# Performance work log

Hardware: AMD Instinct MI355X
Metric: run time of the kernel (lower is better)

## Reference

```python
import jax, jax.numpy as jnp
import numpy as np


def setup_inputs() -> dict:
    key = jax.random.key(0)
    k1, k2 = jax.random.split(key)
    x = jax.random.normal(k1, (64, 3, 512, 512), dtype=jnp.float32)
    mean_params = jax.random.normal(k2, (64, 4), dtype=jnp.float32)
    return {"x": x, "mean_params": mean_params}


def _make_affine(mean_params):
    # 4-param branch: theta, scale, tx, ty -> [B, 2, 3] affine matrices
    theta = mean_params[:, 0]
    scale = mean_params[:, 1]
    tx = mean_params[:, 2]
    ty = mean_params[:, 3]
    ct = scale * jnp.cos(theta)
    st = scale * jnp.sin(theta)
    row0 = jnp.stack([ct, -st, tx], axis=-1)
    row1 = jnp.stack([st, ct, ty], axis=-1)
    return jnp.stack([row0, row1], axis=-2)  # [B, 2, 3]


def _affine_grid(A, H, W):
    # torch.F.affine_grid with align_corners=False base coordinates
    xs = (2.0 * jnp.arange(W, dtype=jnp.float32) + 1.0) / W - 1.0  # [W]
    ys = (2.0 * jnp.arange(H, dtype=jnp.float32) + 1.0) / H - 1.0  # [H]
    # grid_x[b,h,w] = a*x + b*y + c ; grid_y similarly
    gx = (A[:, 0, 0, None, None] * xs[None, None, :]
          + A[:, 0, 1, None, None] * ys[None, :, None]
          + A[:, 0, 2, None, None])  # [B,H,W]
    gy = (A[:, 1, 0, None, None] * xs[None, None, :]
          + A[:, 1, 1, None, None] * ys[None, :, None]
          + A[:, 1, 2, None, None])  # [B,H,W]
    return gx, gy


def _grid_sample(x, gx, gy):
    # bilinear, padding_mode='zeros', align_corners=False (torch defaults)
    B, C, H, W = x.shape
    ix = ((gx + 1.0) * W - 1.0) * 0.5  # [B,H,W] in pixel coords
    iy = ((gy + 1.0) * H - 1.0) * 0.5
    x0f = jnp.floor(ix)
    y0f = jnp.floor(iy)
    fx = ix - x0f
    fy = iy - y0f
    x0 = x0f.astype(jnp.int32)
    y0 = y0f.astype(jnp.int32)
    x1 = x0 + 1
    y1 = y0 + 1

    def gather(yi, xi):
        valid = ((yi >= 0) & (yi < H) & (xi >= 0) & (xi < W))
        yc = jnp.clip(yi, 0, H - 1)
        xc = jnp.clip(xi, 0, W - 1)
        # per-batch gather: img [C,H,W], yc/xc [H,W] -> [C,H,W]
        v = jax.vmap(lambda img, y, xcol: img[:, y, xcol])(x, yc, xc)
        return v * valid[:, None, :, :].astype(x.dtype)

    w00 = ((1.0 - fx) * (1.0 - fy))[:, None]
    w01 = (fx * (1.0 - fy))[:, None]
    w10 = ((1.0 - fx) * fy)[:, None]
    w11 = (fx * fy)[:, None]
    return (w00 * gather(y0, x0) + w01 * gather(y0, x1)
            + w10 * gather(y1, x0) + w11 * gather(y1, x1))


def reference(x, mean_params):
    B, C, H, W = x.shape
    A = _make_affine(mean_params)
    gx, gy = _affine_grid(A, H, W)
    return _grid_sample(x, gx, gy)
```

## Files before the change

kernel.cpp:

```cpp
#include <hip/hip_runtime.h>

#define BB 64
#define CC 3
#define HH 512
#define WW 512
#define HW (HH * WW)
#define CHW (CC * HW)

#define PROWS 64
#define PSTRIDE 68
#define SMEMF (PROWS * PSTRIDE)

typedef float f2_t __attribute__((ext_vector_type(2), aligned(4)));
typedef float f4_t __attribute__((ext_vector_type(4), aligned(16)));

__global__ __launch_bounds__(64) void prep_kernel(const float* __restrict__ mp,
                                                  float4* __restrict__ cf)
{
    int b = threadIdx.x;
    if (b < BB) {
        float theta = mp[b * 4 + 0];
        float scale = mp[b * 4 + 1];
        float tx    = mp[b * 4 + 2];
        float ty    = mp[b * 4 + 3];
        float s, c;
        sincosf(theta, &s, &c);
        float ct = scale * c;
        float st = scale * s;
        const float d = -255.5f;
        float Cx = d * (ct - st) + 256.0f * tx + 255.5f;
        float Cy = d * (st + ct) + 256.0f * ty + 255.5f;
        cf[b] = make_float4(ct, st, Cx, Cy);
    }
}

__global__ __launch_bounds__(256, 8) void affine_sample_kernel(
    const float* __restrict__ x,
    const float4* __restrict__ cf,
    float* __restrict__ out)
{
    __shared__ float smem[SMEMF];

    int tid  = threadIdx.x;
    int lane = tid & 63;
    int wid  = tid >> 6;
    int strip = lane & 7;
    int lrow  = lane >> 3;

    int bidx = blockIdx.x;
    int b    = bidx >> 8;
    int rem  = bidx & 255;
    int tileH = (rem >> 4) << 5;
    int tileW = (rem & 15) << 5;

    int h  = tileH + (wid << 3) + lrow;
    int w0 = tileW + (strip << 2);

    float4 k = cf[b];
    float ct = k.x, st = k.y, Cx = k.z, Cy = k.w;

    float wA = (float)tileW, wB = (float)(tileW + 31);
    float hA = (float)tileH, hB = (float)(tileH + 31);
    float cwA = ct * wA, cwB = ct * wB, shA = st * hA, shB = st * hB;
    float ixmin = fminf(cwA, cwB) - fmaxf(shA, shB) + Cx;
    float ixmax = fmaxf(cwA, cwB) - fminf(shA, shB) + Cx;
    float swA = st * wA, swB = st * wB, chA = ct * hA, chB = ct * hB;
    float iymin = fminf(swA, swB) + fminf(chA, chB) + Cy;
    float iymax = fmaxf(swA, swB) + fmaxf(chA, chB) + Cy;

    int bx_lo = (int)floorf(ixmin) - 1;
    int bx_hi = (int)floorf(ixmax) + 2;
    int by_lo = (int)floorf(iymin) - 1;
    int by_hi = (int)floorf(iymax) + 2;

    float* ob = out + b * CHW + h * WW + w0;

    bool oob = (bx_hi <= 0) | (bx_lo >= WW - 1) | (by_hi <= 0) | (by_lo >= HH - 1);
    if (oob) {
        const f4_t z = {0.0f, 0.0f, 0.0f, 0.0f};
#pragma unroll
        for (int ch = 0; ch < CC; ++ch)
            __builtin_nontemporal_store(z, (f4_t*)(ob + ch * HW));
        return;
    }

    bool interior = (bx_lo >= 0) & (bx_hi <= WW - 1) & (by_lo >= 0) & (by_hi <= HH - 1);

    int px_lo = min(max(bx_lo, 0), WW - 2);
    int px_hi = min(max(bx_hi - 1, 0), WW - 2) + 1;
    int py_lo = min(max(by_lo, 0), HH - 2);
    int py_hi = min(max(by_hi - 1, 0), HH - 2) + 1;
    int By = py_hi - py_lo + 1;

    int ax_lo = px_lo & ~3;
    int span  = px_hi - ax_lo;
    bool staged = (span <= 63) && (By <= PROWS);
    int BxA = (span | 3) + 1;
    if (ax_lo + BxA > WW) ax_lo = WW - BxA;

    int SSTR = BxA + 4;
    int cpc  = By * SSTR;
    bool compact = staged && (3 * cpc <= SMEMF);
    int lstr = compact ? SSTR : PSTRIDE;

    const float* plane0 = x + b * CHW;
    const float* srcb   = plane0 + py_lo * WW + ax_lo;

    int r0 = tid >> 4;
    int c4 = (tid & 15) << 2;

    bool cok = c4 < BxA;
    bool g0 = cok & (r0      < By);
    bool g1 = cok & (r0 + 16 < By);
    bool g2 = cok & (r0 + 32 < By);
    bool g3 = cok & (r0 + 48 < By);

    auto burst = [&](const float* s, float* dst, int stride) {
        f4_t t0 = {0,0,0,0}, t1 = {0,0,0,0}, t2 = {0,0,0,0}, t3 = {0,0,0,0};
        if (g0) t0 = *(const f4_t*)(s +  r0       * WW + c4);
        if (g1) t1 = *(const f4_t*)(s + (r0 + 16) * WW + c4);
        if (g2) t2 = *(const f4_t*)(s + (r0 + 32) * WW + c4);
        if (g3) t3 = *(const f4_t*)(s + (r0 + 48) * WW + c4);
        if (g0) *(f4_t*)(dst +  r0       * stride + c4) = t0;
        if (g1) *(f4_t*)(dst + (r0 + 16) * stride + c4) = t1;
        if (g2) *(f4_t*)(dst + (r0 + 32) * stride + c4) = t2;
        if (g3) *(f4_t*)(dst + (r0 + 48) * stride + c4) = t3;
    };

    float ix = ct * (float)w0 - st * (float)h + Cx;
    float iy = st * (float)w0 + ct * (float)h + Cy;

    float al[4], ar[4], f0[4], f1[4];
    int o0[4], o1[4];

    if (interior) {
#pragma unroll
        for (int p = 0; p < 4; ++p) {
            float x0f = floorf(ix), y0f = floorf(iy);
            float fx = ix - x0f,    fy = iy - y0f;
            int x0 = (int)x0f, y0 = (int)y0f;
            al[p] = 1.0f - fx;
            ar[p] = fx;
            f0[p] = 1.0f - fy;
            f1[p] = fy;
            if (staged) {
                int lx = x0 - ax_lo;
                o0[p] = (y0     - py_lo) * lstr + lx;
                o1[p] = (y0 + 1 - py_lo) * lstr + lx;
            } else {
                o0[p] =  y0      * WW + x0;
                o1[p] = (y0 + 1) * WW + x0;
            }
            ix += ct;
            iy += st;
        }
    } else {
#pragma unroll
        for (int p = 0; p < 4; ++p) {
            float x0f = floorf(ix), y0f = floorf(iy);
            float fx = ix - x0f,    fy = iy - y0f;
            int x0 = (int)x0f, y0 = (int)y0f;
            int y1 = y0 + 1;

            bool xin = (x0 >= 0) & (x0 <= WW - 2);
            float wl = 1.0f - fx;
            al[p] = xin ? wl : ((x0 == -1)     ? fx : 0.0f);
            ar[p] = xin ? fx : ((x0 == WW - 1) ? wl : 0.0f);
            int base = min(max(x0, 0), WW - 2);

            bool vy0 = (y0 >= 0) & (y0 < HH);
            bool vy1 = (y1 >= 0) & (y1 < HH);
            int y0c = min(max(y0, 0), HH - 1);
            int y1c = min(max(y1, 0), HH - 1);
            f0[p] = (1.0f - fy) * (float)vy0;
            f1[p] = fy          * (float)vy1;

            if (staged) {
                int lx = base - ax_lo;
                o0[p] = (y0c - py_lo) * lstr + lx;
                o1[p] = (y1c - py_lo) * lstr + lx;
            } else {
                o0[p] = y0c * WW + base;
                o1[p] = y1c * WW + base;
            }
            ix += ct;
            iy += st;
        }
    }

    if (compact) {
        burst(srcb,          &smem[0],       SSTR);
        burst(srcb + HW,     &smem[cpc],     SSTR);
        burst(srcb + 2 * HW, &smem[2 * cpc], SSTR);
        __syncthreads();
#pragma unroll
        for (int ch = 0; ch < CC; ++ch) {
            const float* pl = &smem[ch * cpc];
            f4_t v;
#pragma unroll
            for (int p = 0; p < 4; ++p) {
                float a0 = pl[o0[p]], a1 = pl[o0[p] + 1];
                float b0 = pl[o1[p]], b1 = pl[o1[p] + 1];
                v[p] = f0[p] * (al[p] * a0 + ar[p] * a1)
                     + f1[p] * (al[p] * b0 + ar[p] * b1);
            }
            __builtin_nontemporal_store(v, (f4_t*)(ob + ch * HW));
        }
    } else if (staged) {
#pragma unroll
        for (int ch = 0; ch < CC; ++ch) {
            if (ch) __syncthreads();
            burst(srcb + ch * HW, smem, PSTRIDE);
            __syncthreads();

            f4_t v;
#pragma unroll
            for (int p = 0; p < 4; ++p) {
                float a0 = smem[o0[p]], a1 = smem[o0[p] + 1];
                float b0 = smem[o1[p]], b1 = smem[o1[p] + 1];
                v[p] = f0[p] * (al[p] * a0 + ar[p] * a1)
                     + f1[p] * (al[p] * b0 + ar[p] * b1);
            }
            __builtin_nontemporal_store(v, (f4_t*)(ob + ch * HW));
        }
    } else {
#pragma unroll
        for (int ch = 0; ch < CC; ++ch) {
            const float* pl = plane0 + ch * HW;
            f4_t v;
#pragma unroll
            for (int p = 0; p < 4; ++p) {
                f2_t t = *(const f2_t*)(pl + o0[p]);
                f2_t u = *(const f2_t*)(pl + o1[p]);
                v[p] = f0[p] * (al[p] * t.x + ar[p] * t.y)
                     + f1[p] * (al[p] * u.x + ar[p] * u.y);
            }
            __builtin_nontemporal_store(v, (f4_t*)(ob + ch * HW));
        }
    }
}

extern "C" void kernel_launch(void* const* d_in, const int* in_sizes, int n_in,
                              void* d_out, int out_size, void* d_ws, size_t ws_size,
                              hipStream_t stream)
{
    const float* x  = (const float*)d_in[0];
    const float* mp = (const float*)d_in[1];
    float* out = (float*)d_out;
    float4* cf = (float4*)d_ws;

    prep_kernel<<<1, 64, 0, stream>>>(mp, cf);
    dim3 block(256);
    dim3 grid(BB * 256);
    affine_sample_kernel<<<grid, block, 0, stream>>>(x, cf, out);
}
```

Baseline: 52.68 us.

## Split unstaged tiles into 16x16 sub-tiles staged through shared memory

When a 32x32 output tile's source footprint is too large to stage, the kernel now processes four 16x16 sub-tiles in turn. Each sub-tile gets its own bounding box, an out-of-bounds zero-store shortcut, and shared-memory staging when the footprint fits. Direct global gathers are kept only as a fallback. This targets scattered uncoalesced gathers for large-scale transforms, at the cost of more barriers and scalar one-pixel-per-thread stores on that path.

```diff
diff --git a/kernel.cpp b/kernel.cpp
--- a/kernel.cpp
+++ b/kernel.cpp
@@ -95,147 +95,241 @@
     int ax_lo = px_lo & ~3;
     int span  = px_hi - ax_lo;
     bool staged = (span <= 63) && (By <= PROWS);
-    int BxA = (span | 3) + 1;
-    if (ax_lo + BxA > WW) ax_lo = WW - BxA;
-
-    int SSTR = BxA + 4;
-    int cpc  = By * SSTR;
-    bool compact = staged && (3 * cpc <= SMEMF);
-    int lstr = compact ? SSTR : PSTRIDE;
 
     const float* plane0 = x + b * CHW;
-    const float* srcb   = plane0 + py_lo * WW + ax_lo;
-
-    int r0 = tid >> 4;
-    int c4 = (tid & 15) << 2;
-
-    bool cok = c4 < BxA;
-    bool g0 = cok & (r0      < By);
-    bool g1 = cok & (r0 + 16 < By);
-    bool g2 = cok & (r0 + 32 < By);
-    bool g3 = cok & (r0 + 48 < By);
-
-    auto burst = [&](const float* s, float* dst, int stride) {
-        f4_t t0 = {0,0,0,0}, t1 = {0,0,0,0}, t2 = {0,0,0,0}, t3 = {0,0,0,0};
-        if (g0) t0 = *(const f4_t*)(s +  r0       * WW + c4);
-        if (g1) t1 = *(const f4_t*)(s + (r0 + 16) * WW + c4);
-        if (g2) t2 = *(const f4_t*)(s + (r0 + 32) * WW + c4);
-        if (g3) t3 = *(const f4_t*)(s + (r0 + 48) * WW + c4);
-        if (g0) *(f4_t*)(dst +  r0       * stride + c4) = t0;
-        if (g1) *(f4_t*)(dst + (r0 + 16) * stride + c4) = t1;
-        if (g2) *(f4_t*)(dst + (r0 + 32) * stride + c4) = t2;
-        if (g3) *(f4_t*)(dst + (r0 + 48) * stride + c4) = t3;
-    };
-
-    float ix = ct * (float)w0 - st * (float)h + Cx;
-    float iy = st * (float)w0 + ct * (float)h + Cy;
-
-    float al[4], ar[4], f0[4], f1[4];
-    int o0[4], o1[4];
-
-    if (interior) {
-#pragma unroll
-        for (int p = 0; p < 4; ++p) {
-            float x0f = floorf(ix), y0f = floorf(iy);
-            float fx = ix - x0f,    fy = iy - y0f;
-            int x0 = (int)x0f, y0 = (int)y0f;
-            al[p] = 1.0f - fx;
-            ar[p] = fx;
-            f0[p] = 1.0f - fy;
-            f1[p] = fy;
-            if (staged) {
+
+    if (staged) {
+        int BxA = (span | 3) + 1;
+        if (ax_lo + BxA > WW) ax_lo = WW - BxA;
+        int SSTR = BxA + 4;
+        int cpc  = By * SSTR;
+        bool compact = (3 * cpc <= SMEMF);
+        int lstr = compact ? SSTR : PSTRIDE;
+
+        const float* srcb = plane0 + py_lo * WW + ax_lo;
+        int r0 = tid >> 4;
+        int c4 = (tid & 15) << 2;
+        bool cok = c4 < BxA;
+        bool g0 = cok & (r0      < By);
+        bool g1 = cok & (r0 + 16 < By);
+        bool g2 = cok & (r0 + 32 < By);
+        bool g3 = cok & (r0 + 48 < By);
+
+        auto burst = [&](const float* s, float* dst, int stride) {
+            f4_t t0 = {0,0,0,0}, t1 = {0,0,0,0}, t2 = {0,0,0,0}, t3 = {0,0,0,0};
+            if (g0) t0 = *(const f4_t*)(s +  r0       * WW + c4);
+            if (g1) t1 = *(const f4_t*)(s + (r0 + 16) * WW + c4);
+            if (g2) t2 = *(const f4_t*)(s + (r0 + 32) * WW + c4);
+            if (g3) t3 = *(const f4_t*)(s + (r0 + 48) * WW + c4);
+            if (g0) *(f4_t*)(dst +  r0       * stride + c4) = t0;
+            if (g1) *(f4_t*)(dst + (r0 + 16) * stride + c4) = t1;
+            if (g2) *(f4_t*)(dst + (r0 + 32) * stride + c4) = t2;
+            if (g3) *(f4_t*)(dst + (r0 + 48) * stride + c4) = t3;
+        };
+
+        float ix = ct * (float)w0 - st * (float)h + Cx;
+        float iy = st * (float)w0 + ct * (float)h + Cy;
+
+        float al[4], ar[4], f0[4], f1[4];
+        int o0[4], o1[4];
+
+        if (interior) {
+#pragma unroll
+            for (int p = 0; p < 4; ++p) {
+                float x0f = floorf(ix), y0f = floorf(iy);
+                float fx = ix - x0f,    fy = iy - y0f;
+                int x0 = (int)x0f, y0 = (int)y0f;
+                al[p] = 1.0f - fx;
+                ar[p] = fx;
+                f0[p] = 1.0f - fy;
+                f1[p] = fy;
                 int lx = x0 - ax_lo;
                 o0[p] = (y0     - py_lo) * lstr + lx;
                 o1[p] = (y0 + 1 - py_lo) * lstr + lx;
-            } else {
-                o0[p] =  y0      * WW + x0;
-                o1[p] = (y0 + 1) * WW + x0;
-            }
-            ix += ct;
-            iy += st;
-        }
-    } else {
-#pragma unroll
-        for (int p = 0; p < 4; ++p) {
-            float x0f = floorf(ix), y0f = floorf(iy);
-            float fx = ix - x0f,    fy = iy - y0f;
-            int x0 = (int)x0f, y0 = (int)y0f;
-            int y1 = y0 + 1;
-
-            bool xin = (x0 >= 0) & (x0 <= WW - 2);
-            float wl = 1.0f - fx;
-            al[p] = xin ? wl : ((x0 == -1)     ? fx : 0.0f);
-            ar[p] = xin ? fx : ((x0 == WW - 1) ? wl : 0.0f);
-            int base = min(max(x0, 0), WW - 2);
-
-            bool vy0 = (y0 >= 0) & (y0 < HH);
-            bool vy1 = (y1 >= 0) & (y1 < HH);
-            int y0c = min(max(y0, 0), HH - 1);
-            int y1c = min(max(y1, 0), HH - 1);
-            f0[p] = (1.0f - fy) * (float)vy0;
-            f1[p] = fy          * (float)vy1;
-
-            if (staged) {
+                ix += ct;
+                iy += st;
+            }
+        } else {
+#pragma unroll
+            for (int p = 0; p < 4; ++p) {
+                float x0f = floorf(ix), y0f = floorf(iy);
+                float fx = ix - x0f,    fy = iy - y0f;
+                int x0 = (int)x0f, y0 = (int)y0f;
+                int y1 = y0 + 1;
+
+                bool xin = (x0 >= 0) & (x0 <= WW - 2);
+                float wl = 1.0f - fx;
+                al[p] = xin ? wl : ((x0 == -1)     ? fx : 0.0f);
+                ar[p] = xin ? fx : ((x0 == WW - 1) ? wl : 0.0f);
+                int base = min(max(x0, 0), WW - 2);
+
+                bool vy0 = (y0 >= 0) & (y0 < HH);
+                bool vy1 = (y1 >= 0) & (y1 < HH);
+                int y0c = min(max(y0, 0), HH - 1);
+                int y1c = min(max(y1, 0), HH - 1);
+                f0[p] = (1.0f - fy) * (float)vy0;
+                f1[p] = fy          * (float)vy1;
+
                 int lx = base - ax_lo;
                 o0[p] = (y0c - py_lo) * lstr + lx;
                 o1[p] = (y1c - py_lo) * lstr + lx;
-            } else {
-                o0[p] = y0c * WW + base;
-                o1[p] = y1c * WW + base;
-            }
-            ix += ct;
-            iy += st;
+                ix += ct;
+                iy += st;
+            }
         }
+
+        if (compact) {
+            burst(srcb,          &smem[0],       SSTR);
+            burst(srcb + HW,     &smem[cpc],     SSTR);
+            burst(srcb + 2 * HW, &smem[2 * cpc], SSTR);
+            __syncthreads();
+#pragma unroll
+            for (int ch = 0; ch < CC; ++ch) {
+                const float* pl = &smem[ch * cpc];
+                f4_t v;
+#pragma unroll
+                for (int p = 0; p < 4; ++p) {
+                    float a0 = pl[o0[p]], a1 = pl[o0[p] + 1];
+                    float b0 = pl[o1[p]], b1 = pl[o1[p] + 1];
+                    v[p] = f0[p] * (al[p] * a0 + ar[p] * a1)
+                         + f1[p] * (al[p] * b0 + ar[p] * b1);
+                }
+                __builtin_nontemporal_store(v, (f4_t*)(ob + ch * HW));
+            }
+        } else {
+#pragma unroll
+            for (int ch = 0; ch < CC; ++ch) {
+                if (ch) __syncthreads();
+                burst(srcb + ch * HW, smem, PSTRIDE);
+                __syncthreads();
+
+                f4_t v;
+#pragma unroll
+                for (int p = 0; p < 4; ++p) {
+                    float a0 = smem[o0[p]], a1 = smem[o0[p] + 1];
+                    float b0 = smem[o1[p]], b1 = smem[o1[p] + 1];
+                    v[p] = f0[p] * (al[p] * a0 + ar[p] * a1)
+                         + f1[p] * (al[p] * b0 + ar[p] * b1);
+                }
+                __builtin_nontemporal_store(v, (f4_t*)(ob + ch * HW));
+            }
+        }
+        return;
     }
 
-    if (compact) {
-        burst(srcb,          &smem[0],       SSTR);
-        burst(srcb + HW,     &smem[cpc],     SSTR);
-        burst(srcb + 2 * HW, &smem[2 * cpc], SSTR);
-        __syncthreads();
-#pragma unroll
-        for (int ch = 0; ch < CC; ++ch) {
-            const float* pl = &smem[ch * cpc];
-            f4_t v;
-#pragma unroll
-            for (int p = 0; p < 4; ++p) {
-                float a0 = pl[o0[p]], a1 = pl[o0[p] + 1];
-                float b0 = pl[o1[p]], b1 = pl[o1[p] + 1];
-                v[p] = f0[p] * (al[p] * a0 + ar[p] * a1)
-                     + f1[p] * (al[p] * b0 + ar[p] * b1);
-            }
-            __builtin_nontemporal_store(v, (f4_t*)(ob + ch * HW));
+    int rS = tid >> 4;
+    int cS = tid & 15;
+    int c4 = cS << 2;
+
+#pragma unroll 1
+    for (int s = 0; s < 4; ++s) {
+        int sW = tileW + ((s & 1) << 4);
+        int sH = tileH + ((s >> 1) << 4);
+
+        float wAs = (float)sW, wBs = (float)(sW + 15);
+        float hAs = (float)sH, hBs = (float)(sH + 15);
+        float cwAs = ct * wAs, cwBs = ct * wBs, shAs = st * hAs, shBs = st * hBs;
+        float ixmn = fminf(cwAs, cwBs) - fmaxf(shAs, shBs) + Cx;
+        float ixmx = fmaxf(cwAs, cwBs) - fminf(shAs, shBs) + Cx;
+        float swAs = st * wAs, swBs = st * wBs, chAs = ct * hAs, chBs = ct * hBs;
+        float iymn = fminf(swAs, swBs) + fminf(chAs, chBs) + Cy;
+        float iymx = fmaxf(swAs, swBs) + fmaxf(chAs, chBs) + Cy;
+
+        int bxl = (int)floorf(ixmn) - 1;
+        int bxh = (int)floorf(ixmx) + 2;
+        int byl = (int)floorf(iymn) - 1;
+        int byh = (int)floorf(iymx) + 2;
+
+        int ws = sW + cS;
+        int hs = sH + rS;
+        float* ob2 = out + b * CHW + hs * WW + ws;
+
+        bool oob_s = (bxh <= 0) | (bxl >= WW - 1) | (byh <= 0) | (byl >= HH - 1);
+        if (oob_s) {
+#pragma unroll
+            for (int ch = 0; ch < CC; ++ch)
+                __builtin_nontemporal_store(0.0f, ob2 + ch * HW);
+            continue;
         }
-    } else if (staged) {
-#pragma unroll
-        for (int ch = 0; ch < CC; ++ch) {
-            if (ch) __syncthreads();
-            burst(srcb + ch * HW, smem, PSTRIDE);
-            __syncthreads();
-
-            f4_t v;
-#pragma unroll
-            for (int p = 0; p < 4; ++p) {
-                float a0 = smem[o0[p]], a1 = smem[o0[p] + 1];
-                float b0 = smem[o1[p]], b1 = smem[o1[p] + 1];
-                v[p] = f0[p] * (al[p] * a0 + ar[p] * a1)
-                     + f1[p] * (al[p] * b0 + ar[p] * b1);
-            }
-            __builtin_nontemporal_store(v, (f4_t*)(ob + ch * HW));
-        }
-    } else {
-#pragma unroll
-        for (int ch = 0; ch < CC; ++ch) {
-            const float* pl = plane0 + ch * HW;
-            f4_t v;
-#pragma unroll
-            for (int p = 0; p < 4; ++p) {
-                f2_t t = *(const f2_t*)(pl + o0[p]);
-                f2_t u = *(const f2_t*)(pl + o1[p]);
-                v[p] = f0[p] * (al[p] * t.x + ar[p] * t.y)
-                     + f1[p] * (al[p] * u.x + ar[p] * u.y);
-            }
-            __builtin_nontemporal_store(v, (f4_t*)(ob + ch * HW));
+
+        int pxl = min(max(bxl, 0), WW - 2);
+        int pxh = min(max(bxh - 1, 0), WW - 2) + 1;
+        int pyl = min(max(byl, 0), HH - 2);
+        int pyh = min(max(byh - 1, 0), HH - 2) + 1;
+        int Bys = pyh - pyl + 1;
+
+        int axl = pxl & ~3;
+        int spn = pxh - axl;
+        bool subok = (spn <= 63) && (Bys <= PROWS);
+        int BxS = (spn | 3) + 1;
+        if (axl + BxS > WW) axl = WW - BxS;
+
+        float ixs = ct * (float)ws - st * (float)hs + Cx;
+        float iys = st * (float)ws + ct * (float)hs + Cy;
+        float x0f = floorf(ixs), y0f = floorf(iys);
+        float fxs = ixs - x0f,   fys = iys - y0f;
+        int x0 = (int)x0f, y0 = (int)y0f;
+        int y1 = y0 + 1;
+
+        bool xin = (x0 >= 0) & (x0 <= WW - 2);
+        float wl = 1.0f - fxs;
+        float alS = xin ? wl  : ((x0 == -1)     ? fxs : 0.0f);
+        float arS = xin ? fxs : ((x0 == WW - 1) ? wl  : 0.0f);
+        int base = min(max(x0, 0), WW - 2);
+
+        bool vy0 = (y0 >= 0) & (y0 < HH);
+        bool vy1 = (y1 >= 0) & (y1 < HH);
+        int y0c = min(max(y0, 0), HH - 1);
+        int y1c = min(max(y1, 0), HH - 1);
+        float f0S = (1.0f - fys) * (float)vy0;
+        float f1S = fys          * (float)vy1;
+
+        if (subok) {
+            int lx  = base - axl;
+            int os0 = (y0c - pyl) * PSTRIDE + lx;
+            int os1 = (y1c - pyl) * PSTRIDE + lx;
+            const float* sb = plane0 + pyl * WW + axl;
+
+            bool cokS = c4 < BxS;
+            bool h0 = cokS & (rS      < Bys);
+            bool h1 = cokS & (rS + 16 < Bys);
+            bool h2 = cokS & (rS + 32 < Bys);
+            bool h3 = cokS & (rS + 48 < Bys);
+
+            for (int ch = 0; ch < CC; ++ch) {
+                __syncthreads();
+                {
+                    const float* ss = sb + ch * HW;
+                    f4_t t0 = {0,0,0,0}, t1 = {0,0,0,0}, t2 = {0,0,0,0}, t3 = {0,0,0,0};
+                    if (h0) t0 = *(const f4_t*)(ss +  rS       * WW + c4);
+                    if (h1) t1 = *(const f4_t*)(ss + (rS + 16) * WW + c4);
+                    if (h2) t2 = *(const f4_t*)(ss + (rS + 32) * WW + c4);
+                    if (h3) t3 = *(const f4_t*)(ss + (rS + 48) * WW + c4);
+                    if (h0) *(f4_t*)(&smem[ rS       * PSTRIDE + c4]) = t0;
+                    if (h1) *(f4_t*)(&smem[(rS + 16) * PSTRIDE + c4]) = t1;
+                    if (h2) *(f4_t*)(&smem[(rS + 32) * PSTRIDE + c4]) = t2;
+                    if (h3) *(f4_t*)(&smem[(rS + 48) * PSTRIDE + c4]) = t3;
+                }
+                __syncthreads();
+
+                float a0 = smem[os0], a1 = smem[os0 + 1];
+                float b0 = smem[os1], b1 = smem[os1 + 1];
+                float v = f0S * (alS * a0 + arS * a1)
+                        + f1S * (alS * b0 + arS * b1);
+                __builtin_nontemporal_store(v, ob2 + ch * HW);
+            }
+        } else {
+            int og0 = y0c * WW + base;
+            int og1 = y1c * WW + base;
+#pragma unroll
+            for (int ch = 0; ch < CC; ++ch) {
+                const float* pl = plane0 + ch * HW;
+                f2_t t = *(const f2_t*)(pl + og0);
+                f2_t u = *(const f2_t*)(pl + og1);
+                float v = f0S * (alS * t.x + arS * t.y)
+                        + f1S * (alS * u.x + arS * u.y);
+                __builtin_nontemporal_store(v, ob2 + ch * HW);
+            }
         }
     }
 }
```

New measurement: 52.91 us. About the same (+0.4%).
